# Kernel optimization log

Hardware: AMD Instinct MI355X
Metric: run time of the kernel (lower is better)

The kernel has to match this reference:

```python
import jax, jax.numpy as jnp
import numpy as np

B, D, K = 32768, 1024, 64
N3, N4, N5 = 512, 512, 512


def setup_inputs() -> dict:
    key = jax.random.key(0)
    ks = jax.random.split(key, 10)
    # x in [-1, 1]^D as the docstring states
    x = jax.random.uniform(ks[0], (B, D), dtype=jnp.float32, minval=-1.0, maxval=1.0)
    S = jnp.sort(jax.random.randint(ks[1], (K,), 0, D, dtype=jnp.int32))
    a = jax.random.normal(ks[2], (K,), dtype=jnp.float32)
    b = jax.random.normal(ks[3], (K, K), dtype=jnp.float32)
    idx3 = jax.random.randint(ks[4], (N3, 3), 0, K, dtype=jnp.int32)
    c3 = jax.random.normal(ks[5], (N3,), dtype=jnp.float32)
    idx4 = jax.random.randint(ks[6], (N4, 4), 0, K, dtype=jnp.int32)
    c4 = jax.random.normal(ks[7], (N4,), dtype=jnp.float32)
    idx5 = jax.random.randint(ks[8], (N5, 5), 0, K, dtype=jnp.int32)
    c5 = jax.random.normal(ks[9], (N5,), dtype=jnp.float32)
    return {"x": x, "S": S, "a": a, "b": b, "idx3": idx3, "c3": c3,
            "idx4": idx4, "c4": c4, "idx5": idx5, "c5": c5}


def _monomial_term(xS, idx, c):
    # xS: (B,k); idx: (n,deg); c: (n,) -> (B,)
    # gather -> (B, n, deg), product over monomial factors, weighted sum
    prod = jnp.prod(xS[:, idx], axis=2)  # (B, n)
    return prod @ c


def reference(x, S, a, b, idx3, c3, idx4, c4, idx5, c5):
    xS = x[:, S]                      # (B, k)
    lin = xS @ a                      # (B,)
    # sum_{i<j} b[i,j] xS_i xS_j == einsum with strictly-upper-triangular b
    bu = jnp.triu(b, k=1)             # (k, k)
    quad = jnp.einsum('bi,ij,bj->b', xS, bu, xS)
    out = lin + quad
    out = out + _monomial_term(xS, idx3, c3)
    out = out + _monomial_term(xS, idx4, c4)
    out = out + _monomial_term(xS, idx5, c5)
    return out
```

## Files before the change

kernel.cpp:

```cpp
#include <hip/hip_runtime.h>
#include <hip/hip_fp16.h>
#include <stdint.h>

#define NT 256
#define RPB 32
#define XSTR 80

#define WS_P3   0
#define WS_P4   4096
#define WS_P5   12288
#define WS_BUTH 20480

static __device__ __forceinline__ __half2 H2(unsigned u) {
    return __builtin_bit_cast(__half2, u);
}
static __device__ __forceinline__ unsigned short f2hbits(float f) {
    __half h = __float2half(f);
    return __builtin_bit_cast(unsigned short, h);
}

__global__ void prepack(const float* __restrict__ b,
                        const int* __restrict__ i3, const float* __restrict__ c3,
                        const int* __restrict__ i4, const float* __restrict__ c4,
                        const int* __restrict__ i5, const float* __restrict__ c5,
                        unsigned char* __restrict__ ws)
{
    const int g = blockIdx.x * NT + threadIdx.x;
    if (g < 4096) {
        int j = g >> 6, i = g & 63;
        float v = (i < j) ? b[i * 64 + j] : 0.0f;
        ((unsigned short*)(ws + WS_BUTH))[g] = f2hbits(v);
    }
    if (g < 512) {
        const int slot = (g & 63) * 8 + (g >> 6);
        unsigned o0, o1, o2, o3, o4;
        o0 = (unsigned)i3[3*g+0] * XSTR; o1 = (unsigned)i3[3*g+1] * XSTR; o2 = (unsigned)i3[3*g+2] * XSTR;
        ((uint2*)(ws + WS_P3))[slot] = make_uint2(o0 | (o1 << 16), o2 | ((unsigned)f2hbits(c3[g]) << 16));
        o0 = (unsigned)i4[4*g+0] * XSTR; o1 = (unsigned)i4[4*g+1] * XSTR;
        o2 = (unsigned)i4[4*g+2] * XSTR; o3 = (unsigned)i4[4*g+3] * XSTR;
        ((uint4*)(ws + WS_P4))[slot] = make_uint4(o0 | (o1 << 16), o2 | (o3 << 16), (unsigned)f2hbits(c4[g]), 0u);
        o0 = (unsigned)i5[5*g+0] * XSTR; o1 = (unsigned)i5[5*g+1] * XSTR;
        o2 = (unsigned)i5[5*g+2] * XSTR; o3 = (unsigned)i5[5*g+3] * XSTR;
        o4 = (unsigned)i5[5*g+4] * XSTR;
        ((uint4*)(ws + WS_P5))[slot] = make_uint4(o0 | (o1 << 16), o2 | (o3 << 16), o4 | ((unsigned)f2hbits(c5[g]) << 16), 0u);
    }
}

static __device__ __forceinline__ void qfma(__half2 bb, uint4 xk, __half2 d[4]) {
    d[0] = __hfma2(bb, H2(xk.x), d[0]);
    d[1] = __hfma2(bb, H2(xk.y), d[1]);
    d[2] = __hfma2(bb, H2(xk.z), d[2]);
    d[3] = __hfma2(bb, H2(xk.w), d[3]);
}
static __device__ __forceinline__ void pmul(const uint4& a, __half2 p[4]) {
    p[0] = __hmul2(p[0], H2(a.x));
    p[1] = __hmul2(p[1], H2(a.y));
    p[2] = __hmul2(p[2], H2(a.z));
    p[3] = __hmul2(p[3], H2(a.w));
}
static __device__ __forceinline__ void pacc(__half2 c2, const __half2 p[4], __half2 acc[4]) {
    acc[0] = __hfma2(c2, p[0], acc[0]);
    acc[1] = __hfma2(c2, p[1], acc[1]);
    acc[2] = __hfma2(c2, p[2], acc[2]);
    acc[3] = __hfma2(c2, p[3], acc[3]);
}

__global__ __launch_bounds__(NT, 4)
void poly_main(const float* __restrict__ x, const int* __restrict__ S,
               const float* __restrict__ a,
               const unsigned char* __restrict__ ws, float* __restrict__ out)
{
    __shared__ __align__(16) __half xS[64 * 40];
    __shared__ float red[4][4][8];

    const int tid  = threadIdx.x;
    const int row0 = blockIdx.x * RPB;

    const int rg = tid & 3;
    const int ts = tid >> 2;

    uint2 e3[8];
    uint4 e4[8], e5[8], bw[8];
    {
        const uint4* s3 = (const uint4*)(ws + WS_P3 + ts * 64);
        #pragma unroll
        for (int i = 0; i < 4; ++i) ((uint4*)e3)[i] = s3[i];
        const uint4* s4 = (const uint4*)(ws + WS_P4 + ts * 128);
        #pragma unroll
        for (int i = 0; i < 8; ++i) e4[i] = s4[i];
        const uint4* s5 = (const uint4*)(ws + WS_P5 + ts * 128);
        #pragma unroll
        for (int i = 0; i < 8; ++i) e5[i] = s5[i];
        const uint4* sb = (const uint4*)(ws + WS_BUTH + ts * 128);
        #pragma unroll
        for (int i = 0; i < 8; ++i) bw[i] = sb[i];
    }
    const float av = a[ts];

    {
        const int k = tid & 63, q = tid >> 6;
        const int sk = S[k];
        const float* xc = x + (size_t)row0 * 1024 + sk;
        float v[8];
        #pragma unroll
        for (int m = 0; m < 8; ++m) v[m] = xc[(size_t)(q * 8 + m) * 1024];
        uint4 pk;
        pk.x = __builtin_bit_cast(unsigned, __floats2half2_rn(v[0], v[1]));
        pk.y = __builtin_bit_cast(unsigned, __floats2half2_rn(v[2], v[3]));
        pk.z = __builtin_bit_cast(unsigned, __floats2half2_rn(v[4], v[5]));
        pk.w = __builtin_bit_cast(unsigned, __floats2half2_rn(v[6], v[7]));
        *(uint4*)((char*)xS + k * XSTR + q * 16) = pk;
    }
    __syncthreads();

    const char* xb = (const char*)xS + rg * 16;

    __half2 d[4] = {H2(0u), H2(0u), H2(0u), H2(0u)};
    {
        const int nii = (ts + 7) >> 3;
        #pragma unroll
        for (int g = 0; g < 8; ++g) {
            if (g < nii) {
                uint4 w4 = bw[g];
                const char* xkb = xb + g * 8 * XSTR;
                unsigned pw[4] = {w4.x, w4.y, w4.z, w4.w};
                #pragma unroll
                for (int p = 0; p < 4; ++p) {
                    __half2 blo = __half2half2(__ushort_as_half((unsigned short)(pw[p] & 0xFFFFu)));
                    __half2 bhi = __half2half2(__ushort_as_half((unsigned short)(pw[p] >> 16)));
                    uint4 x0 = *(const uint4*)(xkb + (2 * p + 0) * XSTR);
                    uint4 x1 = *(const uint4*)(xkb + (2 * p + 1) * XSTR);
                    qfma(blo, x0, d);
                    qfma(bhi, x1, d);
                }
            }
        }
    }
    __half2 acc[4];
    {
        __half2 a2 = __half2half2(__float2half(av));
        uint4 xj = *(const uint4*)(xb + ts * XSTR);
        acc[0] = __hmul2(__hadd2(a2, d[0]), H2(xj.x));
        acc[1] = __hmul2(__hadd2(a2, d[1]), H2(xj.y));
        acc[2] = __hmul2(__hadd2(a2, d[2]), H2(xj.z));
        acc[3] = __hmul2(__hadd2(a2, d[3]), H2(xj.w));
    }

    #pragma unroll
    for (int m = 0; m < 8; ++m) {
        uint2 p = e3[m];
        uint4 v0 = *(const uint4*)(xb + (p.x & 0xFFFFu));
        uint4 v1 = *(const uint4*)(xb + (p.x >> 16));
        uint4 v2 = *(const uint4*)(xb + (p.y & 0xFFFFu));
        __half2 pr[4] = {H2(v0.x), H2(v0.y), H2(v0.z), H2(v0.w)};
        pmul(v1, pr);
        pmul(v2, pr);
        pacc(__half2half2(__ushort_as_half((unsigned short)(p.y >> 16))), pr, acc);
    }
    #pragma unroll
    for (int m = 0; m < 8; ++m) {
        uint4 p = e4[m];
        uint4 v0 = *(const uint4*)(xb + (p.x & 0xFFFFu));
        uint4 v1 = *(const uint4*)(xb + (p.x >> 16));
        uint4 v2 = *(const uint4*)(xb + (p.y & 0xFFFFu));
        uint4 v3 = *(const uint4*)(xb + (p.y >> 16));
        __half2 pr[4] = {H2(v0.x), H2(v0.y), H2(v0.z), H2(v0.w)};
        pmul(v1, pr);
        pmul(v2, pr);
        pmul(v3, pr);
        pacc(__half2half2(__ushort_as_half((unsigned short)(p.z & 0xFFFFu))), pr, acc);
    }
    #pragma unroll
    for (int m = 0; m < 8; ++m) {
        uint4 p = e5[m];
        uint4 v0 = *(const uint4*)(xb + (p.x & 0xFFFFu));
        uint4 v1 = *(const uint4*)(xb + (p.x >> 16));
        uint4 v2 = *(const uint4*)(xb + (p.y & 0xFFFFu));
        uint4 v3 = *(const uint4*)(xb + (p.y >> 16));
        uint4 v4 = *(const uint4*)(xb + (p.z & 0xFFFFu));
        __half2 pr[4] = {H2(v0.x), H2(v0.y), H2(v0.z), H2(v0.w)};
        pmul(v1, pr);
        pmul(v2, pr);
        pmul(v3, pr);
        pmul(v4, pr);
        pacc(__half2half2(__ushort_as_half((unsigned short)(p.z >> 16))), pr, acc);
    }

    float f[8];
    #pragma unroll
    for (int e = 0; e < 4; ++e) {
        f[2 * e]     = __low2float(acc[e]);
        f[2 * e + 1] = __high2float(acc[e]);
    }
    #pragma unroll
    for (int mask = 4; mask <= 32; mask <<= 1) {
        #pragma unroll
        for (int r = 0; r < 8; ++r) f[r] += __shfl_xor(f[r], mask, 64);
    }
    const int w = tid >> 6, lane = tid & 63;
    if (lane < 4) {
        #pragma unroll
        for (int r = 0; r < 8; ++r) red[w][lane][r] = f[r];
    }
    __syncthreads();
    if (tid < 32) {
        int g = tid >> 3, e = tid & 7;
        out[row0 + tid] = red[0][g][e] + red[1][g][e] + red[2][g][e] + red[3][g][e];
    }
}

extern "C" void kernel_launch(void* const* d_in, const int* in_sizes, int n_in,
                              void* d_out, int out_size, void* d_ws, size_t ws_size,
                              hipStream_t stream) {
    const float* x  = (const float*)d_in[0];
    const int*   S  = (const int*)d_in[1];
    const float* a  = (const float*)d_in[2];
    const float* b  = (const float*)d_in[3];
    const int*   i3 = (const int*)d_in[4];
    const float* c3 = (const float*)d_in[5];
    const int*   i4 = (const int*)d_in[6];
    const float* c4 = (const float*)d_in[7];
    const int*   i5 = (const int*)d_in[8];
    const float* c5 = (const float*)d_in[9];
    unsigned char* ws = (unsigned char*)d_ws;
    float* out = (float*)d_out;

    prepack<<<16, NT, 0, stream>>>(b, i3, c3, i4, c4, i5, c5, ws);
    poly_main<<<32768 / RPB, NT, 0, stream>>>(x, S, a, ws, out);
}
```

Baseline: 204.9 us.

## Shrink blocks to one wavefront of 8 rows, dropping cross-wave reduction

Each block becomes a single 64-thread wavefront covering 8 rows, so every thread owns one monomial slot for all 8 rows, and the block count grows 4x. The shared-memory cross-wave reduction and second barrier are replaced by a full-wave shuffle reduction, with one thread writing the 8 outputs as float4s. The degree-5 and quadratic coefficient tables are now streamed from global memory inside the loops instead of being preloaded into registers, to cut register pressure. In exchange the packed coefficient tables are reread by 4x as many blocks, and each block's gather of x is narrower.

```diff
diff --git a/kernel.cpp b/kernel.cpp
--- a/kernel.cpp
+++ b/kernel.cpp
@@ -2,9 +2,9 @@
 #include <hip/hip_fp16.h>
 #include <stdint.h>
 
-#define NT 256
-#define RPB 32
-#define XSTR 80
+#define NT 64
+#define RPB 8
+#define XSTR 48
 
 #define WS_P3   0
 #define WS_P4   4096
@@ -25,7 +25,7 @@
                         const int* __restrict__ i5, const float* __restrict__ c5,
                         unsigned char* __restrict__ ws)
 {
-    const int g = blockIdx.x * NT + threadIdx.x;
+    const int g = blockIdx.x * 256 + threadIdx.x;
     if (g < 4096) {
         int j = g >> 6, i = g & 63;
         float v = (i < j) ? b[i * 64 + j] : 0.0f;
@@ -70,66 +70,53 @@
                const float* __restrict__ a,
                const unsigned char* __restrict__ ws, float* __restrict__ out)
 {
-    __shared__ __align__(16) __half xS[64 * 40];
-    __shared__ float red[4][4][8];
+    __shared__ __align__(16) unsigned char xSb[64 * XSTR];
 
     const int tid  = threadIdx.x;
     const int row0 = blockIdx.x * RPB;
 
-    const int rg = tid & 3;
-    const int ts = tid >> 2;
-
     uint2 e3[8];
-    uint4 e4[8], e5[8], bw[8];
-    {
-        const uint4* s3 = (const uint4*)(ws + WS_P3 + ts * 64);
+    uint4 e4[8];
+    {
+        const uint4* s3 = (const uint4*)(ws + WS_P3 + tid * 64);
         #pragma unroll
         for (int i = 0; i < 4; ++i) ((uint4*)e3)[i] = s3[i];
-        const uint4* s4 = (const uint4*)(ws + WS_P4 + ts * 128);
+        const uint4* s4 = (const uint4*)(ws + WS_P4 + tid * 128);
         #pragma unroll
         for (int i = 0; i < 8; ++i) e4[i] = s4[i];
-        const uint4* s5 = (const uint4*)(ws + WS_P5 + ts * 128);
-        #pragma unroll
-        for (int i = 0; i < 8; ++i) e5[i] = s5[i];
-        const uint4* sb = (const uint4*)(ws + WS_BUTH + ts * 128);
-        #pragma unroll
-        for (int i = 0; i < 8; ++i) bw[i] = sb[i];
-    }
-    const float av = a[ts];
-
-    {
-        const int k = tid & 63, q = tid >> 6;
-        const int sk = S[k];
+    }
+    const float av = a[tid];
+
+    {
+        const int sk = S[tid];
         const float* xc = x + (size_t)row0 * 1024 + sk;
         float v[8];
         #pragma unroll
-        for (int m = 0; m < 8; ++m) v[m] = xc[(size_t)(q * 8 + m) * 1024];
+        for (int m = 0; m < 8; ++m) v[m] = xc[(size_t)m * 1024];
         uint4 pk;
         pk.x = __builtin_bit_cast(unsigned, __floats2half2_rn(v[0], v[1]));
         pk.y = __builtin_bit_cast(unsigned, __floats2half2_rn(v[2], v[3]));
         pk.z = __builtin_bit_cast(unsigned, __floats2half2_rn(v[4], v[5]));
         pk.w = __builtin_bit_cast(unsigned, __floats2half2_rn(v[6], v[7]));
-        *(uint4*)((char*)xS + k * XSTR + q * 16) = pk;
+        *(uint4*)(xSb + tid * XSTR) = pk;
     }
     __syncthreads();
 
-    const char* xb = (const char*)xS + rg * 16;
-
     __half2 d[4] = {H2(0u), H2(0u), H2(0u), H2(0u)};
     {
-        const int nii = (ts + 7) >> 3;
+        const uint4* bwp = (const uint4*)(ws + WS_BUTH + tid * 128);
+        const int nii = (tid + 7) >> 3;
         #pragma unroll
         for (int g = 0; g < 8; ++g) {
             if (g < nii) {
-                uint4 w4 = bw[g];
-                const char* xkb = xb + g * 8 * XSTR;
+                uint4 w4 = bwp[g];
                 unsigned pw[4] = {w4.x, w4.y, w4.z, w4.w};
                 #pragma unroll
                 for (int p = 0; p < 4; ++p) {
                     __half2 blo = __half2half2(__ushort_as_half((unsigned short)(pw[p] & 0xFFFFu)));
                     __half2 bhi = __half2half2(__ushort_as_half((unsigned short)(pw[p] >> 16)));
-                    uint4 x0 = *(const uint4*)(xkb + (2 * p + 0) * XSTR);
-                    uint4 x1 = *(const uint4*)(xkb + (2 * p + 1) * XSTR);
+                    uint4 x0 = *(const uint4*)(xSb + (g * 8 + 2 * p + 0) * XSTR);
+                    uint4 x1 = *(const uint4*)(xSb + (g * 8 + 2 * p + 1) * XSTR);
                     qfma(blo, x0, d);
                     qfma(bhi, x1, d);
                 }
@@ -139,7 +126,7 @@
     __half2 acc[4];
     {
         __half2 a2 = __half2half2(__float2half(av));
-        uint4 xj = *(const uint4*)(xb + ts * XSTR);
+        uint4 xj = *(const uint4*)(xSb + tid * XSTR);
         acc[0] = __hmul2(__hadd2(a2, d[0]), H2(xj.x));
         acc[1] = __hmul2(__hadd2(a2, d[1]), H2(xj.y));
         acc[2] = __hmul2(__hadd2(a2, d[2]), H2(xj.z));
@@ -149,9 +136,9 @@
     #pragma unroll
     for (int m = 0; m < 8; ++m) {
         uint2 p = e3[m];
-        uint4 v0 = *(const uint4*)(xb + (p.x & 0xFFFFu));
-        uint4 v1 = *(const uint4*)(xb + (p.x >> 16));
-        uint4 v2 = *(const uint4*)(xb + (p.y & 0xFFFFu));
+        uint4 v0 = *(const uint4*)(xSb + (p.x & 0xFFFFu));
+        uint4 v1 = *(const uint4*)(xSb + (p.x >> 16));
+        uint4 v2 = *(const uint4*)(xSb + (p.y & 0xFFFFu));
         __half2 pr[4] = {H2(v0.x), H2(v0.y), H2(v0.z), H2(v0.w)};
         pmul(v1, pr);
         pmul(v2, pr);
@@ -160,30 +147,33 @@
     #pragma unroll
     for (int m = 0; m < 8; ++m) {
         uint4 p = e4[m];
-        uint4 v0 = *(const uint4*)(xb + (p.x & 0xFFFFu));
-        uint4 v1 = *(const uint4*)(xb + (p.x >> 16));
-        uint4 v2 = *(const uint4*)(xb + (p.y & 0xFFFFu));
-        uint4 v3 = *(const uint4*)(xb + (p.y >> 16));
+        uint4 v0 = *(const uint4*)(xSb + (p.x & 0xFFFFu));
+        uint4 v1 = *(const uint4*)(xSb + (p.x >> 16));
+        uint4 v2 = *(const uint4*)(xSb + (p.y & 0xFFFFu));
+        uint4 v3 = *(const uint4*)(xSb + (p.y >> 16));
         __half2 pr[4] = {H2(v0.x), H2(v0.y), H2(v0.z), H2(v0.w)};
         pmul(v1, pr);
         pmul(v2, pr);
         pmul(v3, pr);
         pacc(__half2half2(__ushort_as_half((unsigned short)(p.z & 0xFFFFu))), pr, acc);
     }
-    #pragma unroll
-    for (int m = 0; m < 8; ++m) {
-        uint4 p = e5[m];
-        uint4 v0 = *(const uint4*)(xb + (p.x & 0xFFFFu));
-        uint4 v1 = *(const uint4*)(xb + (p.x >> 16));
-        uint4 v2 = *(const uint4*)(xb + (p.y & 0xFFFFu));
-        uint4 v3 = *(const uint4*)(xb + (p.y >> 16));
-        uint4 v4 = *(const uint4*)(xb + (p.z & 0xFFFFu));
-        __half2 pr[4] = {H2(v0.x), H2(v0.y), H2(v0.z), H2(v0.w)};
-        pmul(v1, pr);
-        pmul(v2, pr);
-        pmul(v3, pr);
-        pmul(v4, pr);
-        pacc(__half2half2(__ushort_as_half((unsigned short)(p.z >> 16))), pr, acc);
+    {
+        const uint4* p5 = (const uint4*)(ws + WS_P5 + tid * 128);
+        #pragma unroll 4
+        for (int m = 0; m < 8; ++m) {
+            uint4 p = p5[m];
+            uint4 v0 = *(const uint4*)(xSb + (p.x & 0xFFFFu));
+            uint4 v1 = *(const uint4*)(xSb + (p.x >> 16));
+            uint4 v2 = *(const uint4*)(xSb + (p.y & 0xFFFFu));
+            uint4 v3 = *(const uint4*)(xSb + (p.y >> 16));
+            uint4 v4 = *(const uint4*)(xSb + (p.z & 0xFFFFu));
+            __half2 pr[4] = {H2(v0.x), H2(v0.y), H2(v0.z), H2(v0.w)};
+            pmul(v1, pr);
+            pmul(v2, pr);
+            pmul(v3, pr);
+            pmul(v4, pr);
+            pacc(__half2half2(__ushort_as_half((unsigned short)(p.z >> 16))), pr, acc);
+        }
     }
 
     float f[8];
@@ -193,19 +183,13 @@
         f[2 * e + 1] = __high2float(acc[e]);
     }
     #pragma unroll
-    for (int mask = 4; mask <= 32; mask <<= 1) {
+    for (int mask = 1; mask <= 32; mask <<= 1) {
         #pragma unroll
         for (int r = 0; r < 8; ++r) f[r] += __shfl_xor(f[r], mask, 64);
     }
-    const int w = tid >> 6, lane = tid & 63;
-    if (lane < 4) {
-        #pragma unroll
-        for (int r = 0; r < 8; ++r) red[w][lane][r] = f[r];
-    }
-    __syncthreads();
-    if (tid < 32) {
-        int g = tid >> 3, e = tid & 7;
-        out[row0 + tid] = red[0][g][e] + red[1][g][e] + red[2][g][e] + red[3][g][e];
+    if (tid == 0) {
+        *(float4*)(out + row0)     = make_float4(f[0], f[1], f[2], f[3]);
+        *(float4*)(out + row0 + 4) = make_float4(f[4], f[5], f[6], f[7]);
     }
 }
 
@@ -225,6 +209,6 @@
     unsigned char* ws = (unsigned char*)d_ws;
     float* out = (float*)d_out;
 
-    prepack<<<16, NT, 0, stream>>>(b, i3, c3, i4, c4, i5, c5, ws);
+    prepack<<<16, 256, 0, stream>>>(b, i3, c3, i4, c4, i5, c5, ws);
     poly_main<<<32768 / RPB, NT, 0, stream>>>(x, S, a, ws, out);
 }
```

After: 211.9 us. 1.03x slower.
